# Kernel tuning notes

Hardware: AMD Instinct MI355X
Metric: run time of the kernel (lower is better)

Reference implementation:

```python
import jax, jax.numpy as jnp
import numpy as np

B, S, D, H, WINDOW = 2, 2048, 2048, 16, 256
HD = D // H  # head_dim = 128

def setup_inputs() -> dict:
    key = jax.random.key(0)
    ks = jax.random.split(key, 6)
    s = 0.02  # initializer_range-like scale for weights
    return {
        "hidden_states": jax.random.normal(ks[0], (B, S, D), jnp.float32),
        "attention_mask": jnp.ones((B, S), jnp.int32),
        "Wq": jax.random.normal(ks[1], (D, D), jnp.float32) * s,
        "Wk": jax.random.normal(ks[2], (D, D), jnp.float32) * s,
        "Wv": jax.random.normal(ks[3], (D, D), jnp.float32) * s,
        "Wo": jax.random.normal(ks[4], (D, D), jnp.float32) * s,
        "bo": jnp.zeros((D,), jnp.float32),
    }

def reference(hidden_states, attention_mask, Wq, Wk, Wv, Wo, bo):
    # GPT-Neo quirk: query is multiplied by sqrt(head_dim) and then
    # dot_product_attention_weights divides by sqrt(head_dim) -> net UNSCALED scores.
    q = (hidden_states @ Wq).reshape(B, S, H, HD)  # [B,S,H,hd]
    k = (hidden_states @ Wk).reshape(B, S, H, HD)
    v = (hidden_states @ Wv).reshape(B, S, H, HD)

    # local causal mask: attend iff i - window < j <= i
    i = jnp.arange(S)[:, None]
    j = jnp.arange(S)[None, :]
    local_causal = (j <= i) & (j > i - WINDOW)  # [S,S]
    mask = local_causal[None, None] & (attention_mask[:, None, None, :] > 0)  # [B,1,S,S]

    neg = jnp.finfo(jnp.float32).min
    scores = jnp.einsum("bqhd,bkhd->bhqk", q, k)  # [B,H,S,S] unscaled
    scores = jnp.where(mask, scores, neg)
    attn = jax.nn.softmax(scores, axis=-1)

    out = jnp.einsum("bhqk,bkhd->bqhd", attn, v).reshape(B, S, D)
    return out @ Wo + bo
```

## Files before the change

kernel.cpp:

```cpp
#include <hip/hip_runtime.h>

#define B_   2
#define S_   2048
#define D_   2048
#define H_   16
#define HD_  128
#define WIN_ 256
#define M_   (B_ * S_)

typedef float  f32x4  __attribute__((ext_vector_type(4)));
typedef short  s16x8  __attribute__((ext_vector_type(8)));
typedef __bf16 bf16x8 __attribute__((ext_vector_type(8)));
typedef unsigned short ushort_t;

__device__ inline unsigned short f2b(float f) {
  unsigned u = __builtin_bit_cast(unsigned, f);
  u += 0x7fffu + ((u >> 16) & 1u);
  return (unsigned short)(u >> 16);
}
__device__ inline float b2f(unsigned short h) {
  unsigned u = ((unsigned)h) << 16;
  return __builtin_bit_cast(float, u);
}

template <typename T>
__device__ auto mfma_impl(T a, T b, f32x4 c, int)
    -> decltype(__builtin_amdgcn_mfma_f32_16x16x32_bf16(a, b, c, 0, 0, 0)) {
  return __builtin_amdgcn_mfma_f32_16x16x32_bf16(a, b, c, 0, 0, 0);
}
template <typename T>
__device__ f32x4 mfma_impl(T a, T b, f32x4 c, long) {
  return __builtin_amdgcn_mfma_f32_16x16x32_bf16(
      __builtin_bit_cast(bf16x8, a), __builtin_bit_cast(bf16x8, b), c, 0, 0, 0);
}
__device__ inline f32x4 mfma_bf16(s16x8 a, s16x8 b, f32x4 c) {
  return mfma_impl(a, b, c, 0);
}

#if defined(__has_builtin)
#if __has_builtin(__builtin_amdgcn_global_load_lds)
#define HAS_GLL 1
#endif
#endif
#ifndef HAS_GLL
#define HAS_GLL 0
#endif

__device__ inline void gl_lds16(const ushort_t* g, ushort_t* lds_wave_base) {
#if HAS_GLL
  __builtin_amdgcn_global_load_lds(
      (const __attribute__((address_space(1))) unsigned int*)g,
      (__attribute__((address_space(3))) unsigned int*)lds_wave_base, 16, 0, 0);
#else
  const int lane = threadIdx.x & 63;
  *(uint4*)(lds_wave_base + lane * 8) = *(const uint4*)g;
#endif
}

__global__ __launch_bounds__(256) void k_split(const float* __restrict__ x,
                                               ushort_t* __restrict__ hi,
                                               ushort_t* __restrict__ lo, int n) {
  int i = (blockIdx.x * 256 + threadIdx.x) * 4;
  if (i + 3 < n) {
    float4 v = *(const float4*)(x + i);
    ushort4 h, l;
    h.x = f2b(v.x); l.x = f2b(v.x - b2f(h.x));
    h.y = f2b(v.y); l.y = f2b(v.y - b2f(h.y));
    h.z = f2b(v.z); l.z = f2b(v.z - b2f(h.z));
    h.w = f2b(v.w); l.w = f2b(v.w - b2f(h.w));
    *(ushort4*)(hi + i) = h;
    *(ushort4*)(lo + i) = l;
  }
}

__global__ __launch_bounds__(256) void k_transpose4(const float* __restrict__ W0,
                                                    const float* __restrict__ W1,
                                                    const float* __restrict__ W2,
                                                    const float* __restrict__ W3,
                                                    ushort_t* __restrict__ T0h,
                                                    ushort_t* __restrict__ T0l,
                                                    ushort_t* __restrict__ T1h,
                                                    ushort_t* __restrict__ T1l,
                                                    ushort_t* __restrict__ T2h,
                                                    ushort_t* __restrict__ T3h) {
  __shared__ float t[32][33];
  const int z = blockIdx.z;
  const float* W = (z == 0) ? W0 : (z == 1) ? W1 : (z == 2) ? W2 : W3;
  ushort_t* Th = (z == 0) ? T0h : (z == 1) ? T1h : (z == 2) ? T2h : T3h;
  ushort_t* Tl = (z == 0) ? T0l : (z == 1) ? T1l : nullptr;
  int bx = blockIdx.x * 32, by = blockIdx.y * 32;
  int tx = threadIdx.x, ty = threadIdx.y;
#pragma unroll
  for (int r = 0; r < 32; r += 8)
    t[ty + r][tx] = W[(size_t)(by + ty + r) * D_ + bx + tx];
  __syncthreads();
#pragma unroll
  for (int r = 0; r < 32; r += 8) {
    float v = t[tx][ty + r];
    unsigned short h = f2b(v);
    Th[(size_t)(bx + ty + r) * D_ + by + tx] = h;
    if (Tl) Tl[(size_t)(bx + ty + r) * D_ + by + tx] = f2b(v - b2f(h));
  }
}

__global__ __launch_bounds__(256) void k_vtrans(const ushort_t* __restrict__ Vb,
                                                ushort_t* __restrict__ Vt) {
  __shared__ ushort_t t[32][33];
  int bx = blockIdx.x * 32, by = blockIdx.y * 32, b = blockIdx.z;
  int tx = threadIdx.x, ty = threadIdx.y;
#pragma unroll
  for (int r = 0; r < 32; r += 8)
    t[ty + r][tx] = Vb[((size_t)(b * S_ + by + ty + r)) * D_ + bx + tx];
  __syncthreads();
#pragma unroll
  for (int r = 0; r < 32; r += 8)
    Vt[((size_t)(b * D_ + bx + ty + r)) * S_ + by + tx] = t[tx][ty + r];
}


__device__ inline void stage32(const ushort_t* __restrict__ g, int rowbase,
                               ushort_t* ldsTile, int tid) {
  const int rr = tid >> 2;
  const int gs = ((tid & 3) ^ ((rr >> 1) & 3)) * 8;
  gl_lds16(g + (size_t)(rowbase + rr) * D_ + gs,
           ldsTile + rowbase * 32 + (tid >> 6) * 512);
}

__global__ __launch_bounds__(512) void k_qkv(
    const ushort_t* __restrict__ Ah, const ushort_t* __restrict__ Al,
    const ushort_t* __restrict__ WqH, const ushort_t* __restrict__ WqL,
    const ushort_t* __restrict__ WkH, const ushort_t* __restrict__ WvH,
    ushort_t* __restrict__ Qh, ushort_t* __restrict__ Ql,
    ushort_t* __restrict__ Ko, ushort_t* __restrict__ Vo) {
  __shared__ ushort_t As_[4][256 * 32];
  __shared__ ushort_t Bs_[4][256 * 32];
  const int tid = threadIdx.x;
  const int wave = tid >> 6, lane = tid & 63;
  const int quad = lane >> 4, l16 = lane & 15;

  const int lid = blockIdx.y * 24 + blockIdx.x;
  const int nlid = (lid & 7) * 48 + (lid >> 3);
  const int bx = nlid % 24, by = nlid / 24;
  const int m0 = by * 256;
  const int wtype = bx >> 3;
  const int n0 = (bx & 7) * 256;
  const int nseg = (wtype == 0) ? 3 : (wtype == 1) ? 2 : 1;
  const ushort_t* Bh0 = (wtype == 0) ? WqH : (wtype == 1) ? WkH : WvH;
  const int NT = nseg << 6;

  const int wrM = (wave >> 2) * 128;
  const int wcN = (wave & 3) * 64;
  const int koff = (quad ^ ((l16 >> 1) & 3)) * 8;

  {
    const ushort_t* Ap = Ah + (size_t)m0 * D_;
    const ushort_t* Bp = Bh0 + (size_t)n0 * D_;
#pragma unroll
    for (int t = 0; t < 3; ++t) {
      stage32(Ap + t * 32, 0,   &As_[t][0], tid);
      stage32(Ap + t * 32, 128, &As_[t][0], tid);
      stage32(Bp + t * 32, 0,   &Bs_[t][0], tid);
      stage32(Bp + t * 32, 128, &Bs_[t][0], tid);
    }
  }
  asm volatile("s_waitcnt vmcnt(8)" ::: "memory");
  __builtin_amdgcn_s_barrier();
  asm volatile("" ::: "memory");

  f32x4 acc[8][4] = {};
  for (int kt = 0; kt < NT; ++kt) {
    const int st = kt + 3;
    const bool doSt = (st < NT);
    const int cur = kt & 3, sb = st & 3;
    const ushort_t* At = &As_[cur][0];
    const ushort_t* Bt = &Bs_[cur][0];
    ushort_t* Ad = &As_[sb][0];
    ushort_t* Bd = &Bs_[sb][0];
    const ushort_t* Asrc = Ah;
    const ushort_t* Bsrc = Bh0;
    if (doSt) {
      const int sg = st >> 6, so = (st & 63) * 32;
      const ushort_t* Ab = (sg == 1) ? Al : Ah;
      const ushort_t* Bb = (sg == 2) ? WqL : Bh0;
      Asrc = Ab + (size_t)m0 * D_ + so;
      Bsrc = Bb + (size_t)n0 * D_ + so;
    }
    s16x8 bf[4];
    {
      s16x8 af[4];
#pragma unroll
      for (int mt = 0; mt < 4; ++mt)
        af[mt] = *(const s16x8*)(At + (wrM + mt * 16 + l16) * 32 + koff);
#pragma unroll
      for (int nt = 0; nt < 4; ++nt)
        bf[nt] = *(const s16x8*)(Bt + (wcN + nt * 16 + l16) * 32 + koff);
      if (doSt) {
        stage32(Asrc, 0,   Ad, tid);
        stage32(Asrc, 128, Ad, tid);
      }
      asm volatile("s_waitcnt lgkmcnt(0)" ::: "memory");
      __builtin_amdgcn_sched_barrier(0);
      __builtin_amdgcn_s_setprio(1);
#pragma unroll
      for (int mt = 0; mt < 4; ++mt)
#pragma unroll
        for (int nt = 0; nt < 4; ++nt)
          acc[mt][nt] = mfma_bf16(af[mt], bf[nt], acc[mt][nt]);
      __builtin_amdgcn_s_setprio(0);
    }
    {
      s16x8 af[4];
#pragma unroll
      for (int mt = 0; mt < 4; ++mt)
        af[mt] = *(const s16x8*)(At + (wrM + 64 + mt * 16 + l16) * 32 + koff);
      if (doSt) {
        stage32(Bsrc, 0,   Bd, tid);
        stage32(Bsrc, 128, Bd, tid);
      }
      asm volatile("s_waitcnt lgkmcnt(0)" ::: "memory");
      __builtin_amdgcn_sched_barrier(0);
      __builtin_amdgcn_s_setprio(1);
#pragma unroll
      for (int mt = 0; mt < 4; ++mt)
#pragma unroll
        for (int nt = 0; nt < 4; ++nt)
          acc[4 + mt][nt] = mfma_bf16(af[mt], bf[nt], acc[4 + mt][nt]);
      __builtin_amdgcn_s_setprio(0);
      if (doSt)              asm volatile("s_waitcnt vmcnt(8)" ::: "memory");
      else if (kt == NT - 3) asm volatile("s_waitcnt vmcnt(4)" ::: "memory");
      else if (kt == NT - 2) asm volatile("s_waitcnt vmcnt(0)" ::: "memory");
      __builtin_amdgcn_s_barrier();
      asm volatile("" ::: "memory");
    }
  }

#pragma unroll
  for (int a = 0; a < 8; ++a)
#pragma unroll
    for (int nt = 0; nt < 4; ++nt)
#pragma unroll
      for (int r = 0; r < 4; ++r) {
        const int row = m0 + wrM + a * 16 + quad * 4 + r;
        const int col = n0 + wcN + nt * 16 + l16;
        const float v = acc[a][nt][r];
        const size_t idx = (size_t)row * D_ + col;
        if (wtype == 0) {
          unsigned short h = f2b(v);
          Qh[idx] = h;
          Ql[idx] = f2b(v - b2f(h));
        } else if (wtype == 1) {
          Ko[idx] = f2b(v);
        } else {
          Vo[idx] = f2b(v);
        }
      }
}

__device__ inline void stage_chunk(const ushort_t* __restrict__ gbase, int K,
                                   int rowbase, ushort_t* ldsTile, int tid) {
  const int rr = tid >> 3;
  const int gs = ((tid & 7) ^ (rr & 7)) * 8;
  gl_lds16(gbase + (size_t)(rowbase + rr) * K + gs,
           ldsTile + rowbase * 64 + (tid >> 6) * 512);
}

template <int NSEG, int OUT>
__global__ __launch_bounds__(512) void k_gemm8(
    const ushort_t* __restrict__ A0, const ushort_t* __restrict__ A1,
    const ushort_t* __restrict__ A2, const ushort_t* __restrict__ B0,
    const ushort_t* __restrict__ B2, ushort_t* __restrict__ Co,
    ushort_t* __restrict__ Col, float* __restrict__ Cf,
    const float* __restrict__ bias, int M, int N, int K) {
  __shared__ ushort_t As_[3][256 * 64];
  __shared__ ushort_t Bs_[3][128 * 64];
  const int tid = threadIdx.x;
  const int wave = tid >> 6, lane = tid & 63;
  const int quad = lane >> 4, l16 = lane & 15;
  const int m0 = blockIdx.y * 256, n0 = blockIdx.x * 128;
  const int wrM = (wave >> 1) * 64;
  const int wcN = (wave & 1) * 64;
  const int aRowB = (wrM + l16) * 64;
  const int bRowB = (wcN + l16) * 64;
  int ks8[2];
  ks8[0] = ((0 + quad) ^ (l16 & 7)) * 8;
  ks8[1] = ((4 + quad) ^ (l16 & 7)) * 8;
  const int NT = NSEG * 32;

  {
    const ushort_t* Ab0 = A0 + (size_t)m0 * K;
    const ushort_t* Bb0 = B0 + (size_t)n0 * K;
#pragma unroll
    for (int t = 0; t < 2; ++t) {
      const ushort_t* Ab = Ab0 + t * 64;
      const ushort_t* Bb = Bb0 + t * 64;
      stage_chunk(Ab, K, 0,   &As_[t][0], tid);
      stage_chunk(Ab, K, 64,  &As_[t][0], tid);
      stage_chunk(Ab, K, 128, &As_[t][0], tid);
      stage_chunk(Ab, K, 192, &As_[t][0], tid);
      stage_chunk(Bb, K, 0,   &Bs_[t][0], tid);
      stage_chunk(Bb, K, 64,  &Bs_[t][0], tid);
    }
  }
  asm volatile("s_waitcnt vmcnt(6)" ::: "memory");
  __builtin_amdgcn_s_barrier();
  asm volatile("" ::: "memory");

  f32x4 acc[4][4] = {};
  int cur = 0;
  for (int kt = 0; kt < NT; ++kt) {
    const int st = kt + 2;
    const bool doStage = (st < NT);
    int sbuf = cur + 2; if (sbuf >= 3) sbuf -= 3;
    ushort_t* At  = &As_[cur][0];
    ushort_t* Bt  = &Bs_[cur][0];
    ushort_t* Ads = &As_[sbuf][0];
    ushort_t* Bds = &Bs_[sbuf][0];
    const ushort_t* Asb = A0;
    const ushort_t* Bsb = B0;
    if (doStage) {
      const int sg = st >> 5;
      const ushort_t* Ag = A0;
      const ushort_t* Bg = B0;
      if (NSEG >= 2 && sg == 1) Ag = A1;
      if (NSEG == 3 && sg == 2) { Ag = A2; Bg = B2; }
      Asb = Ag + (size_t)m0 * K + (size_t)(st & 31) * 64;
      Bsb = Bg + (size_t)n0 * K + (size_t)(st & 31) * 64;
    }
    s16x8 bf[4][2];
#pragma unroll
    for (int p = 0; p < 2; ++p) {
      s16x8 af[2][2];
#pragma unroll
      for (int i = 0; i < 2; ++i)
#pragma unroll
        for (int s = 0; s < 2; ++s)
          af[i][s] = *(const s16x8*)(At + aRowB + (p * 2 + i) * 1024 + ks8[s]);
      if (p == 0) {
#pragma unroll
        for (int nt = 0; nt < 4; ++nt)
#pragma unroll
          for (int s = 0; s < 2; ++s)
            bf[nt][s] = *(const s16x8*)(Bt + bRowB + nt * 1024 + ks8[s]);
      }
      if (doStage) {
        if (p == 0) {
          stage_chunk(Asb, K, 0,   Ads, tid);
          stage_chunk(Asb, K, 64,  Ads, tid);
          stage_chunk(Asb, K, 128, Ads, tid);
        } else {
          stage_chunk(Asb, K, 192, Ads, tid);
          stage_chunk(Bsb, K, 0,   Bds, tid);
          stage_chunk(Bsb, K, 64,  Bds, tid);
        }
      }
      asm volatile("s_waitcnt lgkmcnt(0)" ::: "memory");
      __builtin_amdgcn_sched_barrier(0);
      __builtin_amdgcn_s_setprio(1);
#pragma unroll
      for (int i = 0; i < 2; ++i)
#pragma unroll
        for (int nt = 0; nt < 4; ++nt)
#pragma unroll
          for (int s = 0; s < 2; ++s)
            acc[p * 2 + i][nt] = mfma_bf16(af[i][s], bf[nt][s], acc[p * 2 + i][nt]);
      __builtin_amdgcn_s_setprio(0);
      if (p == 1) {
        if (doStage) asm volatile("s_waitcnt vmcnt(6)" ::: "memory");
        else         asm volatile("s_waitcnt vmcnt(0)" ::: "memory");
        __builtin_amdgcn_s_barrier();
        asm volatile("" ::: "memory");
      }
    }
    cur = (cur == 2) ? 0 : cur + 1;
  }

#pragma unroll
  for (int mt = 0; mt < 4; ++mt)
#pragma unroll
    for (int nt = 0; nt < 4; ++nt)
#pragma unroll
      for (int r = 0; r < 4; ++r) {
        int row = m0 + wrM + mt * 16 + quad * 4 + r;
        int col = n0 + wcN + nt * 16 + l16;
        float v = acc[mt][nt][r];
        if (OUT == 2) {
          Cf[(size_t)row * N + col] = v + bias[col];
        } else if (OUT == 1) {
          unsigned short h = f2b(v);
          Co[(size_t)row * N + col]  = h;
          Col[(size_t)row * N + col] = f2b(v - b2f(h));
        } else {
          Co[(size_t)row * N + col] = f2b(v);
        }
      }
}

__global__ __launch_bounds__(256) void k_fattn(const ushort_t* __restrict__ Qh,
                                               const ushort_t* __restrict__ Ql,
                                               const ushort_t* __restrict__ Kh,
                                               const ushort_t* __restrict__ Vt,
                                               const int* __restrict__ amask,
                                               ushort_t* __restrict__ AO) {
  __shared__ ushort_t Ksh[64][136];
  __shared__ ushort_t Vs[128][72];
  __shared__ ushort_t ps[4][16][72];
  __shared__ int ams[320];
  const int tid = threadIdx.x;
  const int wave = tid >> 6, lane = tid & 63;
  const int quad = lane >> 4, l16 = lane & 15;
  const int qt = blockIdx.x, h = blockIdx.y, b = blockIdx.z;
  const int q0 = qt * 64;

  for (int x = tid; x < 320; x += 256) {
    int j = q0 - 256 + x;
    ams[x] = (j >= 0) ? amask[b * S_ + j] : 0;
  }

  const int qrowA = q0 + wave * 16 + l16;
  const ushort_t* qbh = Qh + ((size_t)(b * S_ + qrowA) * D_) + h * HD_;
  const ushort_t* qbl = Ql + ((size_t)(b * S_ + qrowA) * D_) + h * HD_;
  s16x8 qh[4], ql[4];
#pragma unroll
  for (int kk = 0; kk < 4; kk++) {
    qh[kk] = *(const s16x8*)(qbh + kk * 32 + quad * 8);
    ql[kk] = *(const s16x8*)(qbl + kk * 32 + quad * 8);
  }

  f32x4 O[8] = {};
  float m_run[4], l_run[4];
#pragma unroll
  for (int r = 0; r < 4; r++) { m_run[r] = -3.0e38f; l_run[r] = 0.f; }

  const int t0 = (qt < 4) ? (4 - qt) : 0;
  for (int t = t0; t < 5; t++) {
    const int kb = q0 - 256 + 64 * t;
    __syncthreads();
    {
      const int key = tid >> 2, dimb = (tid & 3) * 32;
      const ushort_t* kgh = Kh + ((size_t)(b * S_ + kb + key) * D_) + h * HD_ + dimb;
#pragma unroll
      for (int u = 0; u < 4; u++)
        *(uint4*)&Ksh[key][dimb + u * 8] = *(const uint4*)(kgh + u * 8);
      const int hd = tid >> 1, keyb = (tid & 1) * 32;
      const ushort_t* vg = Vt + ((size_t)(b * D_ + h * HD_ + hd) * S_) + kb + keyb;
#pragma unroll
      for (int u = 0; u < 4; u++)
        *(uint4*)&Vs[hd][keyb + u * 8] = *(const uint4*)(vg + u * 8);
    }
    __syncthreads();

    f32x4 sacc[4] = {};
#pragma unroll
    for (int kk = 0; kk < 4; kk++)
#pragma unroll
      for (int nt = 0; nt < 4; nt++) {
        s16x8 kfh = *(const s16x8*)&Ksh[nt * 16 + l16][kk * 32 + quad * 8];
        sacc[nt] = mfma_bf16(qh[kk], kfh, sacc[nt]);
        sacc[nt] = mfma_bf16(ql[kk], kfh, sacc[nt]);
      }

#pragma unroll
    for (int nt = 0; nt < 4; nt++) {
      const int j = kb + nt * 16 + l16;
      const bool amok = ams[64 * t + nt * 16 + l16] != 0;
#pragma unroll
      for (int r = 0; r < 4; r++) {
        const int iq = q0 + wave * 16 + quad * 4 + r;
        const bool ok = amok && (j <= iq) && (j > iq - WIN_);
        if (!ok) sacc[nt][r] = -3.0e38f;
      }
    }
    float mt[4];
#pragma unroll
    for (int r = 0; r < 4; r++) {
      mt[r] = fmaxf(fmaxf(sacc[0][r], sacc[1][r]), fmaxf(sacc[2][r], sacc[3][r]));
      mt[r] = fmaxf(mt[r], __shfl_xor(mt[r], 1));
      mt[r] = fmaxf(mt[r], __shfl_xor(mt[r], 2));
      mt[r] = fmaxf(mt[r], __shfl_xor(mt[r], 4));
      mt[r] = fmaxf(mt[r], __shfl_xor(mt[r], 8));
    }
    float alpha[4], lt[4];
#pragma unroll
    for (int r = 0; r < 4; r++) {
      float mnew = fmaxf(m_run[r], mt[r]);
      alpha[r] = __expf(m_run[r] - mnew);
      m_run[r] = mnew;
      lt[r] = 0.f;
#pragma unroll
      for (int nt = 0; nt < 4; nt++) {
        float s = sacc[nt][r];
        float p = (s > -1.0e30f) ? __expf(s - mnew) : 0.f;
        sacc[nt][r] = p;
        lt[r] += p;
      }
      lt[r] += __shfl_xor(lt[r], 1);
      lt[r] += __shfl_xor(lt[r], 2);
      lt[r] += __shfl_xor(lt[r], 4);
      lt[r] += __shfl_xor(lt[r], 8);
      l_run[r] = l_run[r] * alpha[r] + lt[r];
    }
#pragma unroll
    for (int o = 0; o < 8; o++)
#pragma unroll
      for (int r = 0; r < 4; r++) O[o][r] *= alpha[r];
#pragma unroll
    for (int nt = 0; nt < 4; nt++)
#pragma unroll
      for (int r = 0; r < 4; r++)
        ps[wave][quad * 4 + r][nt * 16 + l16] = f2b(sacc[nt][r]);
    __syncthreads();
#pragma unroll
    for (int kk2 = 0; kk2 < 2; kk2++) {
      s16x8 pf = *(const s16x8*)&ps[wave][l16][kk2 * 32 + quad * 8];
#pragma unroll
      for (int o = 0; o < 8; o++) {
        s16x8 vf = *(const s16x8*)&Vs[o * 16 + l16][kk2 * 32 + quad * 8];
        O[o] = mfma_bf16(pf, vf, O[o]);
      }
    }
  }
#pragma unroll
  for (int r = 0; r < 4; r++) l_run[r] = 1.0f / l_run[r];
#pragma unroll
  for (int o = 0; o < 8; o++)
#pragma unroll
    for (int r = 0; r < 4; r++) {
      int row = q0 + wave * 16 + quad * 4 + r;
      AO[((size_t)(b * S_ + row) * D_) + h * HD_ + o * 16 + l16] = f2b(O[o][r] * l_run[r]);
    }
}

extern "C" void kernel_launch(void* const* d_in, const int* in_sizes, int n_in,
                              void* d_out, int out_size, void* d_ws, size_t ws_size,
                              hipStream_t stream) {
  const float* hs    = (const float*)d_in[0];
  const int*   amask = (const int*)d_in[1];
  const float* Wq    = (const float*)d_in[2];
  const float* Wk    = (const float*)d_in[3];
  const float* Wv    = (const float*)d_in[4];
  const float* Wo    = (const float*)d_in[5];
  const float* bo    = (const float*)d_in[6];
  float* out = (float*)d_out;

  char* p = (char*)d_ws;
  ushort_t* hsHi = (ushort_t*)p; p += (size_t)16 << 20;
  ushort_t* hsLo = (ushort_t*)p; p += (size_t)16 << 20;
  ushort_t* WqTh = (ushort_t*)p; p += (size_t)8 << 20;
  ushort_t* WqTl = (ushort_t*)p; p += (size_t)8 << 20;
  ushort_t* WkTh = (ushort_t*)p; p += (size_t)8 << 20;
  ushort_t* WkTl = (ushort_t*)p; p += (size_t)8 << 20;  (void)WkTl;
  ushort_t* WvTh = (ushort_t*)p; p += (size_t)8 << 20;
  ushort_t* WoTh = (ushort_t*)p; p += (size_t)8 << 20;
  ushort_t* Qhb  = (ushort_t*)p; p += (size_t)16 << 20;
  ushort_t* Qlb  = (ushort_t*)p; p += (size_t)16 << 20;
  ushort_t* Khb  = (ushort_t*)p; p += (size_t)16 << 20;
  ushort_t* Vb   = (ushort_t*)p; p += (size_t)16 << 20;
  ushort_t* Vt   = (ushort_t*)p; p += (size_t)16 << 20;

  k_split<<<M_ * D_ / 1024, 256, 0, stream>>>(hs, hsHi, hsLo, M_ * D_);
  dim3 tb(32, 8), tg4(D_ / 32, D_ / 32, 4);
  k_transpose4<<<tg4, tb, 0, stream>>>(Wq, Wk, Wv, Wo, WqTh, WqTl, WkTh, nullptr, WvTh, WoTh);

  dim3 gq(24, 16);
  k_qkv<<<gq, 512, 0, stream>>>(hsHi, hsLo, WqTh, WqTl, WkTh, WvTh, Qhb, Qlb, Khb, Vb);

  dim3 vg(D_ / 32, S_ / 32, B_);
  k_vtrans<<<vg, tb, 0, stream>>>(Vb, Vt);

  dim3 ag(S_ / 64, H_, B_);
  k_fattn<<<ag, 256, 0, stream>>>(Qhb, Qlb, Khb, Vt, amask, hsHi );

  dim3 gg(D_ / 128, M_ / 256);
  k_gemm8<1, 2><<<gg, 512, 0, stream>>>(hsHi , nullptr, nullptr, WoTh, nullptr,
                                        nullptr, nullptr, out, bo, M_, D_, D_);
}
```

Before: 428.2 us.

## Double-buffer QKV GEMM fragments in registers and deepen global prefetch to four stages

The QKV projection main loop now reads the next k-tile's A/B fragments from LDS into a second register set while MFMAs run on the current set, ping-ponging between two register banks. Global-to-LDS staging goes from three tiles ahead to four, with one barrier per k-tile instead of splitting the tile into two halves that each wait on LDS. The aim is to hide LDS read latency and global load latency behind the MFMA work. The cost is higher VGPR pressure, which could reduce occupancy or cause spills.

```diff
diff --git a/kernel.cpp b/kernel.cpp
--- a/kernel.cpp
+++ b/kernel.cpp
@@ -156,83 +156,80 @@
     const ushort_t* Ap = Ah + (size_t)m0 * D_;
     const ushort_t* Bp = Bh0 + (size_t)n0 * D_;
 #pragma unroll
-    for (int t = 0; t < 3; ++t) {
+    for (int t = 0; t < 4; ++t) {
       stage32(Ap + t * 32, 0,   &As_[t][0], tid);
       stage32(Ap + t * 32, 128, &As_[t][0], tid);
       stage32(Bp + t * 32, 0,   &Bs_[t][0], tid);
       stage32(Bp + t * 32, 128, &Bs_[t][0], tid);
     }
   }
+  asm volatile("s_waitcnt vmcnt(12)" ::: "memory");
+  __builtin_amdgcn_s_barrier();
+  asm volatile("" ::: "memory");
+
+  s16x8 afA[8], bfA[4], afB[8], bfB[4];
+#pragma unroll
+  for (int a = 0; a < 8; ++a)
+    afA[a] = *(const s16x8*)(&As_[0][0] + (wrM + a * 16 + l16) * 32 + koff);
+#pragma unroll
+  for (int nt = 0; nt < 4; ++nt)
+    bfA[nt] = *(const s16x8*)(&Bs_[0][0] + (wcN + nt * 16 + l16) * 32 + koff);
+  asm volatile("s_waitcnt lgkmcnt(0)" ::: "memory");
   asm volatile("s_waitcnt vmcnt(8)" ::: "memory");
   __builtin_amdgcn_s_barrier();
   asm volatile("" ::: "memory");
 
   f32x4 acc[8][4] = {};
-  for (int kt = 0; kt < NT; ++kt) {
-    const int st = kt + 3;
-    const bool doSt = (st < NT);
-    const int cur = kt & 3, sb = st & 3;
-    const ushort_t* At = &As_[cur][0];
-    const ushort_t* Bt = &Bs_[cur][0];
-    ushort_t* Ad = &As_[sb][0];
-    ushort_t* Bd = &Bs_[sb][0];
-    const ushort_t* Asrc = Ah;
-    const ushort_t* Bsrc = Bh0;
-    if (doSt) {
-      const int sg = st >> 6, so = (st & 63) * 32;
-      const ushort_t* Ab = (sg == 1) ? Al : Ah;
-      const ushort_t* Bb = (sg == 2) ? WqL : Bh0;
-      Asrc = Ab + (size_t)m0 * D_ + so;
-      Bsrc = Bb + (size_t)n0 * D_ + so;
-    }
-    s16x8 bf[4];
-    {
-      s16x8 af[4];
-#pragma unroll
-      for (int mt = 0; mt < 4; ++mt)
-        af[mt] = *(const s16x8*)(At + (wrM + mt * 16 + l16) * 32 + koff);
-#pragma unroll
-      for (int nt = 0; nt < 4; ++nt)
-        bf[nt] = *(const s16x8*)(Bt + (wcN + nt * 16 + l16) * 32 + koff);
-      if (doSt) {
-        stage32(Asrc, 0,   Ad, tid);
-        stage32(Asrc, 128, Ad, tid);
-      }
-      asm volatile("s_waitcnt lgkmcnt(0)" ::: "memory");
-      __builtin_amdgcn_sched_barrier(0);
-      __builtin_amdgcn_s_setprio(1);
-#pragma unroll
-      for (int mt = 0; mt < 4; ++mt)
-#pragma unroll
-        for (int nt = 0; nt < 4; ++nt)
-          acc[mt][nt] = mfma_bf16(af[mt], bf[nt], acc[mt][nt]);
-      __builtin_amdgcn_s_setprio(0);
-    }
-    {
-      s16x8 af[4];
-#pragma unroll
-      for (int mt = 0; mt < 4; ++mt)
-        af[mt] = *(const s16x8*)(At + (wrM + 64 + mt * 16 + l16) * 32 + koff);
-      if (doSt) {
-        stage32(Bsrc, 0,   Bd, tid);
-        stage32(Bsrc, 128, Bd, tid);
-      }
-      asm volatile("s_waitcnt lgkmcnt(0)" ::: "memory");
-      __builtin_amdgcn_sched_barrier(0);
-      __builtin_amdgcn_s_setprio(1);
-#pragma unroll
-      for (int mt = 0; mt < 4; ++mt)
-#pragma unroll
-        for (int nt = 0; nt < 4; ++nt)
-          acc[4 + mt][nt] = mfma_bf16(af[mt], bf[nt], acc[4 + mt][nt]);
-      __builtin_amdgcn_s_setprio(0);
-      if (doSt)              asm volatile("s_waitcnt vmcnt(8)" ::: "memory");
-      else if (kt == NT - 3) asm volatile("s_waitcnt vmcnt(4)" ::: "memory");
-      else if (kt == NT - 2) asm volatile("s_waitcnt vmcnt(0)" ::: "memory");
-      __builtin_amdgcn_s_barrier();
-      asm volatile("" ::: "memory");
-    }
-  }
+
+#define QKV_TILE_BODY(AFC, BFC, AFN, BFN)                                      \
+  do {                                                                         \
+    const bool doRd = (kt + 1 < NT);                                           \
+    if (doRd) {                                                                \
+      const ushort_t* Ab = &As_[(kt + 1) & 3][0];                              \
+      const ushort_t* Bb = &Bs_[(kt + 1) & 3][0];                              \
+      _Pragma("unroll") for (int a = 0; a < 8; ++a)                            \
+        AFN[a] = *(const s16x8*)(Ab + (wrM + a * 16 + l16) * 32 + koff);       \
+      _Pragma("unroll") for (int nt = 0; nt < 4; ++nt)                         \
+        BFN[nt] = *(const s16x8*)(Bb + (wcN + nt * 16 + l16) * 32 + koff);     \
+    }                                                                          \
+    {                                                                          \
+      const int st = kt + 4;                                                   \
+      if (st < NT) {                                                           \
+        const int sg = st >> 6, so = (st & 63) * 32;                           \
+        const ushort_t* Asrc = ((sg == 1) ? Al : Ah) + (size_t)m0 * D_ + so;   \
+        const ushort_t* Bsrc = ((sg == 2) ? WqL : Bh0) + (size_t)n0 * D_ + so; \
+        ushort_t* Ad = &As_[kt & 3][0];                                        \
+        ushort_t* Bd = &Bs_[kt & 3][0];                                        \
+        stage32(Asrc, 0, Ad, tid);                                             \
+        stage32(Asrc, 128, Ad, tid);                                           \
+        stage32(Bsrc, 0, Bd, tid);                                             \
+        stage32(Bsrc, 128, Bd, tid);                                           \
+      }                                                                        \
+    }                                                                          \
+    __builtin_amdgcn_sched_barrier(0);                                         \
+    __builtin_amdgcn_s_setprio(1);                                             \
+    _Pragma("unroll") for (int a = 0; a < 8; ++a)                              \
+      _Pragma("unroll") for (int nt = 0; nt < 4; ++nt)                         \
+        acc[a][nt] = mfma_bf16(AFC[a], BFC[nt], acc[a][nt]);                   \
+    __builtin_amdgcn_s_setprio(0);                                             \
+    if (doRd) asm volatile("s_waitcnt lgkmcnt(0)" ::: "memory");               \
+    if (kt <= NT - 5)                                                          \
+      asm volatile("s_waitcnt vmcnt(8)" ::: "memory");                         \
+    else if (kt == NT - 4)                                                     \
+      asm volatile("s_waitcnt vmcnt(4)" ::: "memory");                         \
+    else                                                                       \
+      asm volatile("s_waitcnt vmcnt(0)" ::: "memory");                         \
+    __builtin_amdgcn_s_barrier();                                              \
+    asm volatile("" ::: "memory");                                             \
+    ++kt;                                                                      \
+  } while (0)
+
+  int kt = 0;
+  while (kt < NT) {
+    QKV_TILE_BODY(afA, bfA, afB, bfB);
+    QKV_TILE_BODY(afB, bfB, afA, bfA);
+  }
+#undef QKV_TILE_BODY
 
 #pragma unroll
   for (int a = 0; a < 8; ++a)
```

Measured after the change: 452.8 us. 5.8% more time.

## Restructure QKV GEMM into 64-wide K tiles with eight-phase ping-pong pipeline

Applied to the files above, without the earlier changes.

The QKV projection kernel changes its K-tile width from 32 to 64, going from four 32-wide LDS buffers to two 64-wide ping-pong buffers per operand with a new XOR swizzle. Each pair of K tiles now runs as eight MFMA phases, each bracketed by block barriers, with global-to-LDS staging of the next tiles spread across those phases. The aim is fewer loop iterations and waitcnt points per K and better overlap of loads with MFMA work. In exchange it adds many more s_barrier calls per iteration and a shallower prefetch depth.

```diff
diff --git a/kernel.cpp b/kernel.cpp
--- a/kernel.cpp
+++ b/kernel.cpp
@@ -118,12 +118,12 @@
 }
 
 
-__device__ inline void stage32(const ushort_t* __restrict__ g, int rowbase,
+__device__ inline void stage64(const ushort_t* __restrict__ g, int rowbase,
                                ushort_t* ldsTile, int tid) {
-  const int rr = tid >> 2;
-  const int gs = ((tid & 3) ^ ((rr >> 1) & 3)) * 8;
-  gl_lds16(g + (size_t)(rowbase + rr) * D_ + gs,
-           ldsTile + rowbase * 32 + (tid >> 6) * 512);
+  const int r = tid >> 3;
+  const int gs = ((tid & 7) ^ (r & 7)) * 8;
+  gl_lds16(g + (size_t)(rowbase + r) * D_ + gs,
+           ldsTile + rowbase * 64 + (tid >> 6) * 512);
 }
 
 __global__ __launch_bounds__(512) void k_qkv(
@@ -132,8 +132,8 @@
     const ushort_t* __restrict__ WkH, const ushort_t* __restrict__ WvH,
     ushort_t* __restrict__ Qh, ushort_t* __restrict__ Ql,
     ushort_t* __restrict__ Ko, ushort_t* __restrict__ Vo) {
-  __shared__ ushort_t As_[4][256 * 32];
-  __shared__ ushort_t Bs_[4][256 * 32];
+  __shared__ ushort_t Ab_[2][256 * 64];
+  __shared__ ushort_t Bb_[2][256 * 64];
   const int tid = threadIdx.x;
   const int wave = tid >> 6, lane = tid & 63;
   const int quad = lane >> 4, l16 = lane & 15;
@@ -146,93 +146,220 @@
   const int n0 = (bx & 7) * 256;
   const int nseg = (wtype == 0) ? 3 : (wtype == 1) ? 2 : 1;
   const ushort_t* Bh0 = (wtype == 0) ? WqH : (wtype == 1) ? WkH : WvH;
-  const int NT = nseg << 6;
+  const int NT = nseg << 5;
+  const int NI = NT >> 1;
 
   const int wrM = (wave >> 2) * 128;
   const int wcN = (wave & 3) * 64;
-  const int koff = (quad ^ ((l16 >> 1) & 3)) * 8;
+  const int ko0 = (quad ^ (l16 & 7)) * 8;
+  const int ko1 = ((4 + quad) ^ (l16 & 7)) * 8;
+
+#define SRC_A(t) ((((t) >> 5) == 1 ? Al : Ah) + (size_t)m0 * D_ + ((t) & 31) * 64)
+#define SRC_B(t) ((((t) >> 5) == 2 ? WqL : Bh0) + (size_t)n0 * D_ + ((t) & 31) * 64)
+#define RD(buf, row, ko) (*(const s16x8*)((buf) + (row) * 64 + (ko)))
 
   {
-    const ushort_t* Ap = Ah + (size_t)m0 * D_;
-    const ushort_t* Bp = Bh0 + (size_t)n0 * D_;
-#pragma unroll
-    for (int t = 0; t < 3; ++t) {
-      stage32(Ap + t * 32, 0,   &As_[t][0], tid);
-      stage32(Ap + t * 32, 128, &As_[t][0], tid);
-      stage32(Bp + t * 32, 0,   &Bs_[t][0], tid);
-      stage32(Bp + t * 32, 128, &Bs_[t][0], tid);
-    }
-  }
-  asm volatile("s_waitcnt vmcnt(8)" ::: "memory");
+    const ushort_t* sA0 = SRC_A(0);
+    const ushort_t* sB0 = SRC_B(0);
+    const ushort_t* sB1 = SRC_B(1);
+    stage64(sA0, 0,   &Ab_[0][0], tid); stage64(sA0, 64,  &Ab_[0][0], tid);
+    stage64(sA0, 128, &Ab_[0][0], tid); stage64(sA0, 192, &Ab_[0][0], tid);
+    stage64(sB0, 0,   &Bb_[0][0], tid); stage64(sB0, 64,  &Bb_[0][0], tid);
+    stage64(sB0, 128, &Bb_[0][0], tid); stage64(sB0, 192, &Bb_[0][0], tid);
+    stage64(sB1, 0,   &Bb_[1][0], tid); stage64(sB1, 64,  &Bb_[1][0], tid);
+    stage64(sB1, 128, &Bb_[1][0], tid); stage64(sB1, 192, &Bb_[1][0], tid);
+  }
+  asm volatile("s_waitcnt vmcnt(4)" ::: "memory");
   __builtin_amdgcn_s_barrier();
   asm volatile("" ::: "memory");
 
+#define PH_PRE()                                         \
+  __builtin_amdgcn_s_barrier();                          \
+  asm volatile("s_waitcnt lgkmcnt(0)" ::: "memory");     \
+  __builtin_amdgcn_sched_barrier(0);                     \
+  __builtin_amdgcn_s_setprio(1)
+#define PH_POST()                                        \
+  __builtin_amdgcn_s_setprio(0);                         \
+  __builtin_amdgcn_s_barrier();                          \
+  asm volatile("" ::: "memory")
+
   f32x4 acc[8][4] = {};
-  for (int kt = 0; kt < NT; ++kt) {
-    const int st = kt + 3;
-    const bool doSt = (st < NT);
-    const int cur = kt & 3, sb = st & 3;
-    const ushort_t* At = &As_[cur][0];
-    const ushort_t* Bt = &Bs_[cur][0];
-    ushort_t* Ad = &As_[sb][0];
-    ushort_t* Bd = &Bs_[sb][0];
-    const ushort_t* Asrc = Ah;
-    const ushort_t* Bsrc = Bh0;
+  s16x8 aF[4][2], bL[2][2], bH[2][2];
+
+  for (int i = 0; i < NI; ++i) {
+    const int t0 = 2 * i;
+    const bool doSt = (i + 1 < NI);
+    const ushort_t* A0 = &Ab_[0][0];
+    const ushort_t* B0 = &Bb_[0][0];
+    const ushort_t* A1 = &Ab_[1][0];
+    const ushort_t* B1 = &Bb_[1][0];
+    const ushort_t* sAt1 = SRC_A(t0 + 1);
+    const ushort_t* sAt2 = SRC_A(t0 + 2);
+    const ushort_t* sBt2 = SRC_B(t0 + 2);
+    const ushort_t* sBt3 = SRC_B(t0 + 3);
+
+#pragma unroll
+    for (int f = 0; f < 4; ++f) {
+      aF[f][0] = RD(A0, wrM + f * 16 + l16, ko0);
+      aF[f][1] = RD(A0, wrM + f * 16 + l16, ko1);
+    }
+#pragma unroll
+    for (int c = 0; c < 2; ++c) {
+      bL[c][0] = RD(B0, wcN + c * 16 + l16, ko0);
+      bL[c][1] = RD(B0, wcN + c * 16 + l16, ko1);
+    }
+    stage64(sAt1, 0, &Ab_[1][0], tid);
+    stage64(sAt1, 64, &Ab_[1][0], tid);
+    PH_PRE();
+#pragma unroll
+    for (int f = 0; f < 4; ++f)
+#pragma unroll
+      for (int c = 0; c < 2; ++c) {
+        acc[f][c] = mfma_bf16(aF[f][0], bL[c][0], acc[f][c]);
+        acc[f][c] = mfma_bf16(aF[f][1], bL[c][1], acc[f][c]);
+      }
+    PH_POST();
+
+#pragma unroll
+    for (int c = 0; c < 2; ++c) {
+      bH[c][0] = RD(B0, wcN + 32 + c * 16 + l16, ko0);
+      bH[c][1] = RD(B0, wcN + 32 + c * 16 + l16, ko1);
+    }
+    stage64(sAt1, 128, &Ab_[1][0], tid);
+    stage64(sAt1, 192, &Ab_[1][0], tid);
+    PH_PRE();
+#pragma unroll
+    for (int f = 0; f < 4; ++f)
+#pragma unroll
+      for (int c = 0; c < 2; ++c) {
+        acc[f][2 + c] = mfma_bf16(aF[f][0], bH[c][0], acc[f][2 + c]);
+        acc[f][2 + c] = mfma_bf16(aF[f][1], bH[c][1], acc[f][2 + c]);
+      }
+    PH_POST();
+
+#pragma unroll
+    for (int f = 0; f < 4; ++f) {
+      aF[f][0] = RD(A0, wrM + 64 + f * 16 + l16, ko0);
+      aF[f][1] = RD(A0, wrM + 64 + f * 16 + l16, ko1);
+    }
     if (doSt) {
-      const int sg = st >> 6, so = (st & 63) * 32;
-      const ushort_t* Ab = (sg == 1) ? Al : Ah;
-      const ushort_t* Bb = (sg == 2) ? WqL : Bh0;
-      Asrc = Ab + (size_t)m0 * D_ + so;
-      Bsrc = Bb + (size_t)n0 * D_ + so;
-    }
-    s16x8 bf[4];
-    {
-      s16x8 af[4];
-#pragma unroll
-      for (int mt = 0; mt < 4; ++mt)
-        af[mt] = *(const s16x8*)(At + (wrM + mt * 16 + l16) * 32 + koff);
-#pragma unroll
-      for (int nt = 0; nt < 4; ++nt)
-        bf[nt] = *(const s16x8*)(Bt + (wcN + nt * 16 + l16) * 32 + koff);
-      if (doSt) {
-        stage32(Asrc, 0,   Ad, tid);
-        stage32(Asrc, 128, Ad, tid);
-      }
-      asm volatile("s_waitcnt lgkmcnt(0)" ::: "memory");
-      __builtin_amdgcn_sched_barrier(0);
-      __builtin_amdgcn_s_setprio(1);
-#pragma unroll
-      for (int mt = 0; mt < 4; ++mt)
-#pragma unroll
-        for (int nt = 0; nt < 4; ++nt)
-          acc[mt][nt] = mfma_bf16(af[mt], bf[nt], acc[mt][nt]);
-      __builtin_amdgcn_s_setprio(0);
-    }
-    {
-      s16x8 af[4];
-#pragma unroll
-      for (int mt = 0; mt < 4; ++mt)
-        af[mt] = *(const s16x8*)(At + (wrM + 64 + mt * 16 + l16) * 32 + koff);
-      if (doSt) {
-        stage32(Bsrc, 0,   Bd, tid);
-        stage32(Bsrc, 128, Bd, tid);
-      }
-      asm volatile("s_waitcnt lgkmcnt(0)" ::: "memory");
-      __builtin_amdgcn_sched_barrier(0);
-      __builtin_amdgcn_s_setprio(1);
-#pragma unroll
-      for (int mt = 0; mt < 4; ++mt)
-#pragma unroll
-        for (int nt = 0; nt < 4; ++nt)
-          acc[4 + mt][nt] = mfma_bf16(af[mt], bf[nt], acc[4 + mt][nt]);
-      __builtin_amdgcn_s_setprio(0);
-      if (doSt)              asm volatile("s_waitcnt vmcnt(8)" ::: "memory");
-      else if (kt == NT - 3) asm volatile("s_waitcnt vmcnt(4)" ::: "memory");
-      else if (kt == NT - 2) asm volatile("s_waitcnt vmcnt(0)" ::: "memory");
+      stage64(sBt2, 0, &Bb_[0][0], tid);
+      stage64(sBt2, 64, &Bb_[0][0], tid);
+    }
+    PH_PRE();
+#pragma unroll
+    for (int f = 0; f < 4; ++f)
+#pragma unroll
+      for (int c = 0; c < 2; ++c) {
+        acc[4 + f][c] = mfma_bf16(aF[f][0], bL[c][0], acc[4 + f][c]);
+        acc[4 + f][c] = mfma_bf16(aF[f][1], bL[c][1], acc[4 + f][c]);
+      }
+    PH_POST();
+
+    if (doSt) {
+      stage64(sBt2, 128, &Bb_[0][0], tid);
+      stage64(sBt2, 192, &Bb_[0][0], tid);
+    }
+    PH_PRE();
+#pragma unroll
+    for (int f = 0; f < 4; ++f)
+#pragma unroll
+      for (int c = 0; c < 2; ++c) {
+        acc[4 + f][2 + c] = mfma_bf16(aF[f][0], bH[c][0], acc[4 + f][2 + c]);
+        acc[4 + f][2 + c] = mfma_bf16(aF[f][1], bH[c][1], acc[4 + f][2 + c]);
+      }
+    __builtin_amdgcn_s_setprio(0);
+    if (doSt) asm volatile("s_waitcnt vmcnt(4)" ::: "memory");
+    else      asm volatile("s_waitcnt vmcnt(0)" ::: "memory");
+    __builtin_amdgcn_s_barrier();
+    asm volatile("" ::: "memory");
+
+#pragma unroll
+    for (int f = 0; f < 4; ++f) {
+      aF[f][0] = RD(A1, wrM + f * 16 + l16, ko0);
+      aF[f][1] = RD(A1, wrM + f * 16 + l16, ko1);
+    }
+#pragma unroll
+    for (int c = 0; c < 2; ++c) {
+      bL[c][0] = RD(B1, wcN + c * 16 + l16, ko0);
+      bL[c][1] = RD(B1, wcN + c * 16 + l16, ko1);
+    }
+    if (doSt) {
+      stage64(sAt2, 0, &Ab_[0][0], tid);
+      stage64(sAt2, 64, &Ab_[0][0], tid);
+    }
+    PH_PRE();
+#pragma unroll
+    for (int f = 0; f < 4; ++f)
+#pragma unroll
+      for (int c = 0; c < 2; ++c) {
+        acc[f][c] = mfma_bf16(aF[f][0], bL[c][0], acc[f][c]);
+        acc[f][c] = mfma_bf16(aF[f][1], bL[c][1], acc[f][c]);
+      }
+    PH_POST();
+
+#pragma unroll
+    for (int c = 0; c < 2; ++c) {
+      bH[c][0] = RD(B1, wcN + 32 + c * 16 + l16, ko0);
+      bH[c][1] = RD(B1, wcN + 32 + c * 16 + l16, ko1);
+    }
+    if (doSt) {
+      stage64(sAt2, 128, &Ab_[0][0], tid);
+      stage64(sAt2, 192, &Ab_[0][0], tid);
+    }
+    PH_PRE();
+#pragma unroll
+    for (int f = 0; f < 4; ++f)
+#pragma unroll
+      for (int c = 0; c < 2; ++c) {
+        acc[f][2 + c] = mfma_bf16(aF[f][0], bH[c][0], acc[f][2 + c]);
+        acc[f][2 + c] = mfma_bf16(aF[f][1], bH[c][1], acc[f][2 + c]);
+      }
+    PH_POST();
+
+#pragma unroll
+    for (int f = 0; f < 4; ++f) {
+      aF[f][0] = RD(A1, wrM + 64 + f * 16 + l16, ko0);
+      aF[f][1] = RD(A1, wrM + 64 + f * 16 + l16, ko1);
+    }
+    if (doSt) {
+      stage64(sBt3, 0, &Bb_[1][0], tid);
+      stage64(sBt3, 64, &Bb_[1][0], tid);
+    }
+    PH_PRE();
+#pragma unroll
+    for (int f = 0; f < 4; ++f)
+#pragma unroll
+      for (int c = 0; c < 2; ++c) {
+        acc[4 + f][c] = mfma_bf16(aF[f][0], bL[c][0], acc[4 + f][c]);
+        acc[4 + f][c] = mfma_bf16(aF[f][1], bL[c][1], acc[4 + f][c]);
+      }
+    PH_POST();
+
+    if (doSt) {
+      stage64(sBt3, 128, &Bb_[1][0], tid);
+      stage64(sBt3, 192, &Bb_[1][0], tid);
+    }
+    PH_PRE();
+#pragma unroll
+    for (int f = 0; f < 4; ++f)
+#pragma unroll
+      for (int c = 0; c < 2; ++c) {
+        acc[4 + f][2 + c] = mfma_bf16(aF[f][0], bH[c][0], acc[4 + f][2 + c]);
+        acc[4 + f][2 + c] = mfma_bf16(aF[f][1], bH[c][1], acc[4 + f][2 + c]);
+      }
+    __builtin_amdgcn_s_setprio(0);
+    if (doSt) {
+      asm volatile("s_waitcnt vmcnt(4)" ::: "memory");
       __builtin_amdgcn_s_barrier();
       asm volatile("" ::: "memory");
     }
   }
+#undef PH_PRE
+#undef PH_POST
+#undef SRC_A
+#undef SRC_B
+#undef RD
 
 #pragma unroll
   for (int a = 0; a < 8; ++a)
```

Measured after the change: 426.7 us. No clear change (-0.4%).
